# Kernel tuning notes

Measured on AMD Instinct MI355X. Metric: run time of the kernel, lower is better.

## Reference

```python
import jax, jax.numpy as jnp
import numpy as np


def setup_inputs() -> dict:
    key = jax.random.key(0)
    k0, k1, k2, k3, k4, k5 = jax.random.split(key, 6)
    N, E, F, D, H = 50000, 1000000, 128, 32, 4
    # xavier_normal with gain = calculate_gain('relu') = sqrt(2)
    std = np.sqrt(2.0) * np.sqrt(2.0 / (F + D))
    return {
        "entity_features": jax.random.normal(k0, (N, 1, F), jnp.float32),
        "relation_features": jax.random.normal(k1, (E, 1, F), jnp.float32),
        "src": jax.random.randint(k2, (E,), 0, N, jnp.int32),
        "dst": jax.random.randint(k3, (E,), 0, N, jnp.int32),
        "w_q": jax.random.normal(k4, (H, F, D), jnp.float32) * std,
        "w_k": jax.random.normal(k5, (H, F, D), jnp.float32) * std,
    }


def reference(entity_features, relation_features, src, dst, w_q, w_k):
    # entity_features: (N, 1, F) -> repeat over heads is just a broadcast
    feat = entity_features[:, 0, :]        # (N, F)
    rel = relation_features[:, 0, :]       # (E, F)
    num_heads = w_q.shape[0]
    N = feat.shape[0]

    # per-head projections: q = feat @ w_q, k = feat @ w_k, erel = rel @ w_k
    q = jnp.einsum("nf,hfd->nhd", feat, w_q)      # (N, H, D)  'out_el'
    k = jnp.einsum("nf,hfd->nhd", feat, w_k)      # (N, H, D)  'out_er'
    erel = jnp.einsum("ef,hfd->ehd", rel, w_k)    # (E, H, D)  'out_erel'

    # v_dot_u: dst's out_er . src's out_el ; e_dot_u: edge out_erel . src's out_er
    e = (jnp.einsum("ehd,ehd->eh", k[dst], q[src])
         + jnp.einsum("ehd,ehd->eh", erel, k[src]))   # (E, H)
    e = jax.nn.leaky_relu(e, negative_slope=0.01)

    # edge_softmax normalized by source node (softmax over outgoing edges)
    m = jax.ops.segment_max(e, src, num_segments=N)   # (N, H)
    m = jnp.where(jnp.isfinite(m), m, jnp.zeros_like(m))
    ex = jnp.exp(e - m[src])                          # (E, H)
    denom = jax.ops.segment_sum(ex, src, num_segments=N)  # (N, H)
    att = ex / denom[src]                             # (E, H)

    # squeeze(-1).sum(-1)/num_heads on the (E, H, 1) edge tensor -> mean over heads
    return att.sum(axis=-1) / num_heads               # (E,)
```

## Files before the change

kernel.cpp:

```cpp
#include <hip/hip_runtime.h>

#define HH 4
#define FF 128
#define DD 32

typedef float f32x4 __attribute__((ext_vector_type(4)));
typedef _Float16 h16x4 __attribute__((ext_vector_type(4)));
typedef _Float16 h16x2 __attribute__((ext_vector_type(2)));


__global__ void scatter_kernel(const int* __restrict__ src, const int* __restrict__ dst,
                               int* __restrict__ cursor, int2* __restrict__ ed, int E) {
    int i = blockIdx.x * blockDim.x + threadIdx.x;
    if (i >= E) return;
    int s = src[i];
    int pos = atomicAdd(&cursor[s], 1);
    long long pack = (unsigned)i | ((long long)dst[i] << 32);
    __builtin_nontemporal_store(pack, (long long*)&ed[pos]);
}


__global__ __launch_bounds__(256) void qk_hist_kernel(
    const float* __restrict__ feat, const float* __restrict__ wq,
    const float* __restrict__ wk, _Float16* __restrict__ q,
    _Float16* __restrict__ k, int N,
    const int* __restrict__ src, int* __restrict__ counts, int E, int QKB) {
    __shared__ float fs[32 * FF];
    int bid = blockIdx.x;
    if (bid >= QKB) {
        int i = ((bid - QKB) * 256 + threadIdx.x) * 4;
        if (i + 3 < E) {
            int4 v = *(const int4*)(src + i);
            atomicAdd(&counts[v.x], 1);
            atomicAdd(&counts[v.y], 1);
            atomicAdd(&counts[v.z], 1);
            atomicAdd(&counts[v.w], 1);
        } else {
            for (; i < E; ++i) atomicAdd(&counts[src[i]], 1);
        }
        return;
    }
    int n0 = bid * 32;
    int nb = N - n0; if (nb > 32) nb = 32;
    const float4* s4 = (const float4*)(feat + (size_t)n0 * FF);
    int nf4 = nb * FF / 4;
    for (int i = threadIdx.x; i < nf4; i += 256) ((float4*)fs)[i] = s4[i];
    __syncthreads();

    int half = threadIdx.x >> 7;
    int o    = threadIdx.x & 127;
    int h = o >> 5, d = o & 31;
    const float* wqp = wq + ((size_t)h * FF) * DD + d;
    const float* wkp = wk + ((size_t)h * FF) * DD + d;

    float accq[16], acck[16];
#pragma unroll
    for (int e = 0; e < 16; ++e) { accq[e] = 0.f; acck[e] = 0.f; }
    for (int f = 0; f < FF; f += 4) {
        float wq0 = wqp[(f + 0) * DD], wq1 = wqp[(f + 1) * DD];
        float wq2 = wqp[(f + 2) * DD], wq3 = wqp[(f + 3) * DD];
        float wk0 = wkp[(f + 0) * DD], wk1 = wkp[(f + 1) * DD];
        float wk2 = wkp[(f + 2) * DD], wk3 = wkp[(f + 3) * DD];
#pragma unroll
        for (int e = 0; e < 16; ++e) {
            float4 fv = *(const float4*)&fs[(half * 16 + e) * FF + f];
            accq[e] += fv.x * wq0 + fv.y * wq1 + fv.z * wq2 + fv.w * wq3;
            acck[e] += fv.x * wk0 + fv.y * wk1 + fv.z * wk2 + fv.w * wk3;
        }
    }
    int ecnt = nb - half * 16; if (ecnt < 0) ecnt = 0; if (ecnt > 16) ecnt = 16;
    for (int e = 0; e < ecnt; ++e) {
        size_t n = (size_t)(n0 + half * 16 + e);
        q[(n * HH + h) * DD + d] = (_Float16)accq[e];
        k[(n * HH + h) * DD + d] = (_Float16)acck[e];
    }
}


__global__ __launch_bounds__(256) void kk_alloc_kernel(
    const _Float16* __restrict__ kbuf, const float* __restrict__ wk,
    _Float16* __restrict__ kkout, int N,
    const int* __restrict__ counts, int* __restrict__ startb,
    int* __restrict__ cursor, int* __restrict__ gcur, int KKB) {
    __shared__ float ks[16 * FF];
    int bid = blockIdx.x;
    if (bid >= KKB) {
        int sid = (bid - KKB) * 256 + threadIdx.x;
        int lane = threadIdx.x & 63;
        int cnt = (sid < N) ? counts[sid] : 0;
        int incl = cnt;
#pragma unroll
        for (int off = 1; off < 64; off <<= 1) {
            int y = __shfl_up(incl, off, 64);
            if (lane >= off) incl += y;
        }
        int total = __shfl(incl, 63, 64);
        int base = 0;
        if (lane == 63) base = atomicAdd(gcur, total);
        base = __shfl(base, 63, 64);
        if (sid < N) {
            int st = base + incl - cnt;
            startb[sid] = st;
            cursor[sid] = st;
        }
        return;
    }
    int n0 = bid * 16;
    int nb = N - n0; if (nb > 16) nb = 16;
    const h16x4* s4 = (const h16x4*)(kbuf + (size_t)n0 * FF);
    int nh4 = nb * FF / 4;
    for (int i = threadIdx.x; i < nh4; i += 256) {
        h16x4 v = s4[i];
        ((float4*)ks)[i] = make_float4((float)v.x, (float)v.y, (float)v.z, (float)v.w);
    }
    __syncthreads();

    int o = threadIdx.x;
    int h1 = o >> 7, f1 = o & 127;
    int h2 = h1 + 2;
    const float* w1 = wk + ((size_t)h1 * FF + f1) * DD;
    const float* w2 = wk + ((size_t)h2 * FF + f1) * DD;

    float acc1[16], acc2[16];
#pragma unroll
    for (int e = 0; e < 16; ++e) { acc1[e] = 0.f; acc2[e] = 0.f; }
    for (int d = 0; d < DD; d += 4) {
        float4 wv1 = *(const float4*)&w1[d];
        float4 wv2 = *(const float4*)&w2[d];
#pragma unroll
        for (int e = 0; e < 16; ++e) {
            float4 k1 = *(const float4*)&ks[e * FF + h1 * DD + d];
            float4 k2 = *(const float4*)&ks[e * FF + h2 * DD + d];
            acc1[e] += k1.x * wv1.x + k1.y * wv1.y + k1.z * wv1.z + k1.w * wv1.w;
            acc2[e] += k2.x * wv2.x + k2.y * wv2.y + k2.z * wv2.z + k2.w * wv2.w;
        }
    }
    for (int e = 0; e < nb; ++e) {
        kkout[((size_t)(n0 + e) * HH + h1) * FF + f1] = (_Float16)acc1[e];
        kkout[((size_t)(n0 + e) * HH + h2) * FF + f1] = (_Float16)acc2[e];
    }
}


__device__ __forceinline__ void score_row(
    const float* __restrict__ rel, const _Float16* __restrict__ k,
    int e_i, int dd, int t,
    const float4* kkA, const float4* kkB, const float2* qv, float* ev) {
    const float* rp = rel + (size_t)e_i * FF + t * 8;
    f32x4 r0 = __builtin_nontemporal_load((const f32x4*)rp);
    f32x4 r1 = __builtin_nontemporal_load((const f32x4*)(rp + 4));
#pragma unroll
    for (int h = 0; h < HH; ++h) {
        h16x2 kvh = *(const h16x2*)(k + ((size_t)dd * HH + h) * DD + t * 2);
        float a = r0.x * kkA[h].x + r0.y * kkA[h].y + r0.z * kkA[h].z + r0.w * kkA[h].w
                + r1.x * kkB[h].x + r1.y * kkB[h].y + r1.z * kkB[h].z + r1.w * kkB[h].w
                + qv[h].x * (float)kvh.x + qv[h].y * (float)kvh.y;
#pragma unroll
        for (int off = 1; off < 16; off <<= 1) a += __shfl_xor(a, off, 64);
        ev[h] = a >= 0.f ? a : 0.01f * a;
    }
}

__global__ __launch_bounds__(256) void group_kernel(
    const float* __restrict__ rel, const int2* __restrict__ ed,
    const _Float16* __restrict__ q, const _Float16* __restrict__ k,
    const _Float16* __restrict__ kk, const int* __restrict__ start,
    const int* __restrict__ counts, float* __restrict__ out, int N) {
    __shared__ __align__(16) float e_buf_all[4][128][4];
    int wid = threadIdx.x >> 6;
    int s = blockIdx.x * 4 + wid;
    if (s >= N) return;
    int cnt = counts[s];
    if (cnt == 0) return;
    int base = start[s];
    int lane = threadIdx.x & 63;
    int g = lane >> 4, t = lane & 15;
    int hsel = ((t & 1) << 1) | ((t & 2) >> 1);
    float (*e_buf)[4] = e_buf_all[wid];

    float4 kkA[HH], kkB[HH];
    float2 qv[HH];
    const _Float16* kkbase = kk + (size_t)s * (HH * FF) + t * 8;
    const _Float16* qbase  = q  + (size_t)s * (HH * DD) + t * 2;
#pragma unroll
    for (int h = 0; h < HH; ++h) {
        h16x4 a = *(const h16x4*)(kkbase + h * FF);
        h16x4 b = *(const h16x4*)(kkbase + h * FF + 4);
        kkA[h] = make_float4((float)a.x, (float)a.y, (float)a.z, (float)a.w);
        kkB[h] = make_float4((float)b.x, (float)b.y, (float)b.z, (float)b.w);
        h16x2 qh = *(const h16x2*)(qbase + h * DD);
        qv[h] = make_float2((float)qh.x, (float)qh.y);
    }

    float mloc = -INFINITY;
    bool fast = (cnt <= 128);

    for (int c0 = 0; c0 < cnt; c0 += 64) {
        int nc = min(cnt - c0, 64);
        int pv = 0, dv = 0;
        if (lane < nc) { int2 pd = ed[base + c0 + lane]; pv = pd.x; dv = pd.y; }
        for (int j0 = 0; j0 < nc; j0 += 4) {
            int idx = j0 + g;
            int sel = idx < nc ? idx : 0;
            int e_i = __shfl(pv, sel, 64);
            int dd  = __shfl(dv, sel, 64);
            const float* rp = rel + (size_t)e_i * FF + t * 8;
            f32x4 r0 = __builtin_nontemporal_load((const f32x4*)rp);
            f32x4 r1 = __builtin_nontemporal_load((const f32x4*)(rp + 4));
            float p[HH];
#pragma unroll
            for (int h = 0; h < HH; ++h) {
                h16x2 kvh = *(const h16x2*)(k + ((size_t)dd * HH + h) * DD + t * 2);
                p[h] = r0.x * kkA[h].x + r0.y * kkA[h].y + r0.z * kkA[h].z + r0.w * kkA[h].w
                     + r1.x * kkB[h].x + r1.y * kkB[h].y + r1.z * kkB[h].z + r1.w * kkB[h].w
                     + qv[h].x * (float)kvh.x + qv[h].y * (float)kvh.y;
            }
            float sx = (t & 1) ? p[0] : p[2];
            float sy = (t & 1) ? p[1] : p[3];
            float rx = __shfl_xor(sx, 1, 64);
            float ry = __shfl_xor(sy, 1, 64);
            float a0 = ((t & 1) ? p[2] : p[0]) + rx;
            float a1 = ((t & 1) ? p[3] : p[1]) + ry;
            float sz = (t & 2) ? a0 : a1;
            float rz = __shfl_xor(sz, 2, 64);
            float e = ((t & 2) ? a1 : a0) + rz;
            e += __shfl_xor(e, 4, 64);
            e += __shfl_xor(e, 8, 64);
            e = e >= 0.f ? e : 0.01f * e;
            if (idx < nc) {
                mloc = fmaxf(mloc, e);
                if (fast && t < 4) e_buf[c0 + idx][hsel] = e;
            }
        }
    }
    mloc = fmaxf(mloc, __shfl_xor(mloc, 16, 64));
    mloc = fmaxf(mloc, __shfl_xor(mloc, 32, 64));
    float m[HH];
    m[0] = __shfl(mloc, 0, 64);
    m[1] = __shfl(mloc, 2, 64);
    m[2] = __shfl(mloc, 1, 64);
    m[3] = __shfl(mloc, 3, 64);

    if (fast) {
        int i0 = lane, i1 = lane + 64;
        float ex0[HH] = {0.f, 0.f, 0.f, 0.f}, ex1[HH] = {0.f, 0.f, 0.f, 0.f};
        if (i0 < cnt) {
            float4 ev = *(const float4*)e_buf[i0];
            ex0[0] = __expf(ev.x - m[0]); ex0[1] = __expf(ev.y - m[1]);
            ex0[2] = __expf(ev.z - m[2]); ex0[3] = __expf(ev.w - m[3]);
        }
        if (i1 < cnt) {
            float4 ev = *(const float4*)e_buf[i1];
            ex1[0] = __expf(ev.x - m[0]); ex1[1] = __expf(ev.y - m[1]);
            ex1[2] = __expf(ev.z - m[2]); ex1[3] = __expf(ev.w - m[3]);
        }
        float rl[HH];
#pragma unroll
        for (int h = 0; h < HH; ++h) {
            float v = ex0[h] + ex1[h];
#pragma unroll
            for (int off = 1; off < 64; off <<= 1) v += __shfl_xor(v, off, 64);
            rl[h] = 1.0f / v;
        }
        if (i0 < cnt)
            out[ed[base + i0].x] = 0.25f * (ex0[0]*rl[0] + ex0[1]*rl[1] + ex0[2]*rl[2] + ex0[3]*rl[3]);
        if (i1 < cnt)
            out[ed[base + i1].x] = 0.25f * (ex1[0]*rl[0] + ex1[1]*rl[1] + ex1[2]*rl[2] + ex1[3]*rl[3]);
    } else {
        float lacc[HH] = {0.f, 0.f, 0.f, 0.f};
        for (int c0 = 0; c0 < cnt; c0 += 64) {
            int nc = min(cnt - c0, 64);
            int pv = 0, dv = 0;
            if (lane < nc) { int2 pd = ed[base + c0 + lane]; pv = pd.x; dv = pd.y; }
            for (int j0 = 0; j0 < nc; j0 += 4) {
                int idx = j0 + g;
                int sel = idx < nc ? idx : 0;
                int e_i = __shfl(pv, sel, 64);
                int dd  = __shfl(dv, sel, 64);
                float ev[HH];
                score_row(rel, k, e_i, dd, t, kkA, kkB, qv, ev);
                if (idx < nc && t == 0) {
#pragma unroll
                    for (int h = 0; h < HH; ++h) lacc[h] += __expf(ev[h] - m[h]);
                }
            }
        }
        float rl[HH];
#pragma unroll
        for (int h = 0; h < HH; ++h) {
            float v = lacc[h];
#pragma unroll
            for (int off = 1; off < 64; off <<= 1) v += __shfl_xor(v, off, 64);
            rl[h] = 1.0f / v;
        }
        for (int c0 = 0; c0 < cnt; c0 += 64) {
            int nc = min(cnt - c0, 64);
            int pv = 0, dv = 0;
            if (lane < nc) { int2 pd = ed[base + c0 + lane]; pv = pd.x; dv = pd.y; }
            for (int j0 = 0; j0 < nc; j0 += 4) {
                int idx = j0 + g;
                int sel = idx < nc ? idx : 0;
                int e_i = __shfl(pv, sel, 64);
                int dd  = __shfl(dv, sel, 64);
                float ev[HH];
                score_row(rel, k, e_i, dd, t, kkA, kkB, qv, ev);
                if (idx < nc && t == 0) {
                    float a = __expf(ev[0]-m[0])*rl[0] + __expf(ev[1]-m[1])*rl[1]
                            + __expf(ev[2]-m[2])*rl[2] + __expf(ev[3]-m[3])*rl[3];
                    out[e_i] = 0.25f * a;
                }
            }
        }
    }
}

extern "C" void kernel_launch(void* const* d_in, const int* in_sizes, int n_in,
                              void* d_out, int out_size, void* d_ws, size_t ws_size,
                              hipStream_t stream) {
    const float* feat = (const float*)d_in[0];
    const float* rel  = (const float*)d_in[1];
    const int*   src  = (const int*)d_in[2];
    const int*   dst  = (const int*)d_in[3];
    const float* wq   = (const float*)d_in[4];
    const float* wk   = (const float*)d_in[5];
    float* out = (float*)d_out;

    const int N = in_sizes[0] / FF;
    const int E = in_sizes[2];

    _Float16* q   = (_Float16*)d_ws;
    _Float16* k   = q  + (size_t)N * HH * DD;
    _Float16* kk  = k  + (size_t)N * HH * DD;
    int* counts   = (int*)(kk + (size_t)N * HH * FF);
    int* gcur     = counts + N;
    int* start    = gcur + 2;
    int* cursor   = start + N;
    int2* ed      = (int2*)(cursor + N);

    int nb  = (N + 255) / 256;
    int QKB = (N + 31) / 32;
    int HB  = (E + 1023) / 1024;
    int KKB = (N + 15) / 16;

    hipMemsetAsync(counts, 0, (size_t)(N + 2) * sizeof(int), stream);
    qk_hist_kernel<<<QKB + HB, 256, 0, stream>>>(feat, wq, wk, q, k, N, src, counts, E, QKB);
    kk_alloc_kernel<<<KKB + nb, 256, 0, stream>>>(k, wk, kk, N, counts, start, cursor, gcur, KKB);
    scatter_kernel<<<(E + 255) / 256, 256, 0, stream>>>(src, dst, cursor, ed, E);
    group_kernel<<<(N + 3) / 4, 256, 0, stream>>>(rel, ed, q, k, kk, start, counts, out, N);
}
```

Measured before the change: 389.8 us.

## Use MFMA fp16 matrix instructions for Q/K and KK node projections

```diff
diff --git a/kernel.cpp b/kernel.cpp
--- a/kernel.cpp
+++ b/kernel.cpp
@@ -5,8 +5,25 @@
 #define DD 32
 
 typedef float f32x4 __attribute__((ext_vector_type(4)));
+typedef _Float16 h16x8 __attribute__((ext_vector_type(8)));
 typedef _Float16 h16x4 __attribute__((ext_vector_type(4)));
 typedef _Float16 h16x2 __attribute__((ext_vector_type(2)));
+
+
+__global__ __launch_bounds__(256) void prep_kernel(
+    const float* __restrict__ wq, const float* __restrict__ wk,
+    _Float16* __restrict__ wqT, _Float16* __restrict__ wkT,
+    _Float16* __restrict__ wkD, int* __restrict__ counts, int N) {
+    int i = blockIdx.x * 256 + threadIdx.x;
+    if (i < 16384) {
+        int c = i >> 7, f = i & 127;
+        int h = c >> 5, d = c & 31;
+        wqT[i] = (_Float16)wq[h * 4096 + f * 32 + d];
+        wkT[i] = (_Float16)wk[h * 4096 + f * 32 + d];
+        wkD[i] = (_Float16)wk[i];
+    }
+    if (i < N + 2) counts[i] = 0;
+}
 
 
 __global__ void scatter_kernel(const int* __restrict__ src, const int* __restrict__ dst,
@@ -20,12 +37,11 @@
 }
 
 
-__global__ __launch_bounds__(256) void qk_hist_kernel(
-    const float* __restrict__ feat, const float* __restrict__ wq,
-    const float* __restrict__ wk, _Float16* __restrict__ q,
-    _Float16* __restrict__ k, int N,
+__global__ __launch_bounds__(256) void qk_mfma_hist(
+    const float* __restrict__ feat, const _Float16* __restrict__ wqT,
+    const _Float16* __restrict__ wkT, _Float16* __restrict__ q16,
+    _Float16* __restrict__ k16, int N,
     const int* __restrict__ src, int* __restrict__ counts, int E, int QKB) {
-    __shared__ float fs[32 * FF];
     int bid = blockIdx.x;
     if (bid >= QKB) {
         int i = ((bid - QKB) * 256 + threadIdx.x) * 4;
@@ -40,49 +56,51 @@
         }
         return;
     }
-    int n0 = bid * 32;
-    int nb = N - n0; if (nb > 32) nb = 32;
-    const float4* s4 = (const float4*)(feat + (size_t)n0 * FF);
-    int nf4 = nb * FF / 4;
-    for (int i = threadIdx.x; i < nf4; i += 256) ((float4*)fs)[i] = s4[i];
-    __syncthreads();
-
-    int half = threadIdx.x >> 7;
-    int o    = threadIdx.x & 127;
-    int h = o >> 5, d = o & 31;
-    const float* wqp = wq + ((size_t)h * FF) * DD + d;
-    const float* wkp = wk + ((size_t)h * FF) * DD + d;
-
-    float accq[16], acck[16];
-#pragma unroll
-    for (int e = 0; e < 16; ++e) { accq[e] = 0.f; acck[e] = 0.f; }
-    for (int f = 0; f < FF; f += 4) {
-        float wq0 = wqp[(f + 0) * DD], wq1 = wqp[(f + 1) * DD];
-        float wq2 = wqp[(f + 2) * DD], wq3 = wqp[(f + 3) * DD];
-        float wk0 = wkp[(f + 0) * DD], wk1 = wkp[(f + 1) * DD];
-        float wk2 = wkp[(f + 2) * DD], wk3 = wkp[(f + 3) * DD];
-#pragma unroll
-        for (int e = 0; e < 16; ++e) {
-            float4 fv = *(const float4*)&fs[(half * 16 + e) * FF + f];
-            accq[e] += fv.x * wq0 + fv.y * wq1 + fv.z * wq2 + fv.w * wq3;
-            acck[e] += fv.x * wk0 + fv.y * wk1 + fv.z * wk2 + fv.w * wk3;
-        }
-    }
-    int ecnt = nb - half * 16; if (ecnt < 0) ecnt = 0; if (ecnt > 16) ecnt = 16;
-    for (int e = 0; e < ecnt; ++e) {
-        size_t n = (size_t)(n0 + half * 16 + e);
-        q[(n * HH + h) * DD + d] = (_Float16)accq[e];
-        k[(n * HH + h) * DD + d] = (_Float16)acck[e];
+    int wid = threadIdx.x >> 6, lane = threadIdx.x & 63;
+    int n0 = bid * 64 + wid * 16;
+    if (n0 >= N) return;
+    int lrow = lane & 15, lk = lane >> 4;
+    int arow = n0 + lrow; if (arow >= N) arow = N - 1;
+
+    f32x4 accq[8], acck[8];
+#pragma unroll
+    for (int t = 0; t < 8; ++t) { accq[t] = (f32x4){0.f,0.f,0.f,0.f}; acck[t] = (f32x4){0.f,0.f,0.f,0.f}; }
+
+#pragma unroll
+    for (int ks = 0; ks < 4; ++ks) {
+        const float* ap = feat + (size_t)arow * FF + ks * 32 + lk * 8;
+        h16x8 a;
+#pragma unroll
+        for (int j = 0; j < 8; ++j) a[j] = (_Float16)ap[j];
+#pragma unroll
+        for (int t = 0; t < 8; ++t) {
+            const _Float16* bq = wqT + (size_t)(t * 16 + lrow) * FF + ks * 32 + lk * 8;
+            const _Float16* bk = wkT + (size_t)(t * 16 + lrow) * FF + ks * 32 + lk * 8;
+            h16x8 b1 = *(const h16x8*)bq;
+            h16x8 b2 = *(const h16x8*)bk;
+            accq[t] = __builtin_amdgcn_mfma_f32_16x16x32_f16(a, b1, accq[t], 0, 0, 0);
+            acck[t] = __builtin_amdgcn_mfma_f32_16x16x32_f16(a, b2, acck[t], 0, 0, 0);
+        }
+    }
+#pragma unroll
+    for (int r = 0; r < 4; ++r) {
+        int n = n0 + lk * 4 + r;
+        if (n < N) {
+#pragma unroll
+            for (int t = 0; t < 8; ++t) {
+                q16[(size_t)n * FF + t * 16 + lrow] = (_Float16)accq[t][r];
+                k16[(size_t)n * FF + t * 16 + lrow] = (_Float16)acck[t][r];
+            }
+        }
     }
 }
 
 
 __global__ __launch_bounds__(256) void kk_alloc_kernel(
-    const _Float16* __restrict__ kbuf, const float* __restrict__ wk,
-    _Float16* __restrict__ kkout, int N,
+    const _Float16* __restrict__ k16, const _Float16* __restrict__ wkD,
+    _Float16* __restrict__ kk16, int N,
     const int* __restrict__ counts, int* __restrict__ startb,
     int* __restrict__ cursor, int* __restrict__ gcur, int KKB) {
-    __shared__ float ks[16 * FF];
     int bid = blockIdx.x;
     if (bid >= KKB) {
         int sid = (bid - KKB) * 256 + threadIdx.x;
@@ -105,39 +123,32 @@
         }
         return;
     }
-    int n0 = bid * 16;
-    int nb = N - n0; if (nb > 16) nb = 16;
-    const h16x4* s4 = (const h16x4*)(kbuf + (size_t)n0 * FF);
-    int nh4 = nb * FF / 4;
-    for (int i = threadIdx.x; i < nh4; i += 256) {
-        h16x4 v = s4[i];
-        ((float4*)ks)[i] = make_float4((float)v.x, (float)v.y, (float)v.z, (float)v.w);
-    }
-    __syncthreads();
-
-    int o = threadIdx.x;
-    int h1 = o >> 7, f1 = o & 127;
-    int h2 = h1 + 2;
-    const float* w1 = wk + ((size_t)h1 * FF + f1) * DD;
-    const float* w2 = wk + ((size_t)h2 * FF + f1) * DD;
-
-    float acc1[16], acc2[16];
-#pragma unroll
-    for (int e = 0; e < 16; ++e) { acc1[e] = 0.f; acc2[e] = 0.f; }
-    for (int d = 0; d < DD; d += 4) {
-        float4 wv1 = *(const float4*)&w1[d];
-        float4 wv2 = *(const float4*)&w2[d];
-#pragma unroll
-        for (int e = 0; e < 16; ++e) {
-            float4 k1 = *(const float4*)&ks[e * FF + h1 * DD + d];
-            float4 k2 = *(const float4*)&ks[e * FF + h2 * DD + d];
-            acc1[e] += k1.x * wv1.x + k1.y * wv1.y + k1.z * wv1.z + k1.w * wv1.w;
-            acc2[e] += k2.x * wv2.x + k2.y * wv2.y + k2.z * wv2.z + k2.w * wv2.w;
-        }
-    }
-    for (int e = 0; e < nb; ++e) {
-        kkout[((size_t)(n0 + e) * HH + h1) * FF + f1] = (_Float16)acc1[e];
-        kkout[((size_t)(n0 + e) * HH + h2) * FF + f1] = (_Float16)acc2[e];
+    int wid = threadIdx.x >> 6, lane = threadIdx.x & 63;
+    int n0 = bid * 64 + wid * 16;
+    if (n0 >= N) return;
+    int lrow = lane & 15, lk = lane >> 4;
+    int arow = n0 + lrow; if (arow >= N) arow = N - 1;
+
+#pragma unroll
+    for (int h = 0; h < HH; ++h) {
+        h16x8 a = *(const h16x8*)(k16 + (size_t)arow * FF + h * 32 + lk * 8);
+        f32x4 acc[8];
+#pragma unroll
+        for (int t = 0; t < 8; ++t) acc[t] = (f32x4){0.f,0.f,0.f,0.f};
+#pragma unroll
+        for (int t = 0; t < 8; ++t) {
+            h16x8 b = *(const h16x8*)(wkD + (size_t)h * 4096 + (size_t)(t * 16 + lrow) * 32 + lk * 8);
+            acc[t] = __builtin_amdgcn_mfma_f32_16x16x32_f16(a, b, acc[t], 0, 0, 0);
+        }
+#pragma unroll
+        for (int r = 0; r < 4; ++r) {
+            int n = n0 + lk * 4 + r;
+            if (n < N) {
+#pragma unroll
+                for (int t = 0; t < 8; ++t)
+                    kk16[(size_t)n * 512 + h * FF + t * 16 + lrow] = (_Float16)acc[t][r];
+            }
+        }
     }
 }
 
@@ -328,23 +339,27 @@
     const int N = in_sizes[0] / FF;
     const int E = in_sizes[2];
 
-    _Float16* q   = (_Float16*)d_ws;
-    _Float16* k   = q  + (size_t)N * HH * DD;
-    _Float16* kk  = k  + (size_t)N * HH * DD;
-    int* counts   = (int*)(kk + (size_t)N * HH * FF);
-    int* gcur     = counts + N;
-    int* start    = gcur + 2;
-    int* cursor   = start + N;
-    int2* ed      = (int2*)(cursor + N);
-
-    int nb  = (N + 255) / 256;
-    int QKB = (N + 31) / 32;
-    int HB  = (E + 1023) / 1024;
-    int KKB = (N + 15) / 16;
-
-    hipMemsetAsync(counts, 0, (size_t)(N + 2) * sizeof(int), stream);
-    qk_hist_kernel<<<QKB + HB, 256, 0, stream>>>(feat, wq, wk, q, k, N, src, counts, E, QKB);
-    kk_alloc_kernel<<<KKB + nb, 256, 0, stream>>>(k, wk, kk, N, counts, start, cursor, gcur, KKB);
+    _Float16* q16  = (_Float16*)d_ws;
+    _Float16* k16  = q16 + (size_t)N * FF;
+    _Float16* kk16 = k16 + (size_t)N * FF;
+    _Float16* wqT  = kk16 + (size_t)N * 512;
+    _Float16* wkT  = wqT + 16384;
+    _Float16* wkD  = wkT + 16384;
+    int* counts    = (int*)(wkD + 16384);
+    int* gcur      = counts + N;
+    int* start     = gcur + 2;
+    int* cursor    = start + N;
+    int2* ed       = (int2*)(cursor + N);
+
+    int nb   = (N + 255) / 256;
+    int QKB  = (N + 63) / 64;
+    int HB   = (E + 1023) / 1024;
+    int KKB  = (N + 63) / 64;
+    int PREP = 16384 > N + 2 ? (16384 + 255) / 256 : (N + 2 + 255) / 256;
+
+    prep_kernel<<<PREP, 256, 0, stream>>>(wq, wk, wqT, wkT, wkD, counts, N);
+    qk_mfma_hist<<<QKB + HB, 256, 0, stream>>>(feat, wqT, wkT, q16, k16, N, src, counts, E, QKB);
+    kk_alloc_kernel<<<KKB + nb, 256, 0, stream>>>(k16, wkD, kk16, N, counts, start, cursor, gcur, KKB);
     scatter_kernel<<<(E + 255) / 256, 256, 0, stream>>>(src, dst, cursor, ed, E);
-    group_kernel<<<(N + 3) / 4, 256, 0, stream>>>(rel, ed, q, k, kk, start, counts, out, N);
-}
+    group_kernel<<<(N + 3) / 4, 256, 0, stream>>>(rel, ed, q16, k16, kk16, start, counts, out, N);
+}
```

Result: faster. 337.1 us (-13.5%).
